# Performance work log

Hardware: AMD Instinct MI355X
Metric: run time of the kernel (lower is better)

## Reference

```python
import math
import jax, jax.numpy as jnp
import numpy as np

NUM_HEADS = 16
HEAD_DIM = 64
NB_FEATURES = 256
EPS = 1e-06
DATA_NORM = HEAD_DIM ** (-0.25)


def setup_inputs() -> dict:
    key = jax.random.key(0)
    ks = jax.random.split(key, 5)
    B, N, C = 4, 4096, 1024
    x = jax.random.normal(ks[0], (B, N, C), dtype=jnp.float32)
    w_qkv = jax.random.normal(ks[1], (C, 3 * C), dtype=jnp.float32) * (C ** -0.5)
    b_qkv = jnp.zeros((3 * C,), dtype=jnp.float32)
    w_out = jax.random.normal(ks[2], (C, C), dtype=jnp.float32) * (C ** -0.5)
    b_out = jnp.zeros((C,), dtype=jnp.float32)
    proj = jax.random.normal(ks[3], (NUM_HEADS, NB_FEATURES, HEAD_DIM), dtype=jnp.float32)
    proj = proj / jnp.linalg.norm(proj, axis=-1, keepdims=True)  # F.normalize(dim=-1)
    return {"x": x, "w_qkv": w_qkv, "b_qkv": b_qkv, "w_out": w_out, "b_out": b_out,
            "proj_matrix": proj}


def _feature_map(x, proj):
    # x: [b,h,n,d], proj: [h,m,d] -> [b,h,n,m]
    x = x * DATA_NORM
    x_proj = jnp.einsum('bhnd,hmd->bhnm', x, proj)
    sq_norms = 0.5 * jnp.sum(x * x, axis=-1, keepdims=True)
    x_proj = x_proj - sq_norms
    x_proj = x_proj - jnp.max(x_proj, axis=-1, keepdims=True)
    return (jnp.exp(x_proj) + EPS) / math.sqrt(NB_FEATURES)


def reference(x, w_qkv, b_qkv, w_out, b_out, proj_matrix):
    B, N, C = x.shape
    h, d = NUM_HEADS, HEAD_DIM
    qkv = x @ w_qkv + b_qkv                     # [B,N,3C]
    q, k, v = jnp.split(qkv, 3, axis=-1)
    to_heads = lambda z: z.reshape(B, N, h, d).transpose(0, 2, 1, 3)  # [B,h,N,d]
    q, k, v = to_heads(q), to_heads(k), to_heads(v)

    q_prime = _feature_map(q, proj_matrix)      # [B,h,N,m]
    k_prime = _feature_map(k, proj_matrix)      # [B,h,N,m]

    k_sum = jnp.sum(k_prime, axis=2)                          # [B,h,m]
    kv = jnp.einsum('bhnm,bhnd->bhmd', k_prime, v)            # [B,h,m,d]
    numerator = jnp.einsum('bhnm,bhmd->bhnd', q_prime, kv)    # [B,h,N,d]
    denominator = jnp.einsum('bhnm,bhm->bhn', q_prime, k_sum) + EPS
    out = numerator / denominator[..., None]

    out = out.transpose(0, 2, 1, 3).reshape(B, N, C)
    return out @ w_out + b_out
```

## Files before the change

kernel.cpp:

```cpp
#include <hip/hip_runtime.h>
#include <hip/hip_bf16.h>
#include <stdint.h>


#define DN 0.35355339059327379f
#define EPSF 1e-6f
#define INV_SQRT_M 0.0625f

typedef __attribute__((ext_vector_type(8))) short bf16x8;
typedef __attribute__((ext_vector_type(4))) float f32x4;

static __device__ __forceinline__ short f2bf(float f) {
    __hip_bfloat16 h = __float2bfloat16(f);
    return *(short*)&h;
}
static __device__ __forceinline__ void gload16(const void* g, void* l) {
    __builtin_amdgcn_global_load_lds(
        (const __attribute__((address_space(1))) void*)g,
        (__attribute__((address_space(3))) void*)l,
        16, 0, 0);
}

__global__ __launch_bounds__(256) void conv_x(const float* __restrict__ X,
                                              short* __restrict__ Xb) {
    int i = blockIdx.x * 256 + threadIdx.x;
    float4 v = ((const float4*)X)[i];
    short4 o;
    o.x = f2bf(v.x); o.y = f2bf(v.y); o.z = f2bf(v.z); o.w = f2bf(v.w);
    ((short4*)Xb)[i] = o;
}

__global__ __launch_bounds__(256) void convt_w(const float* __restrict__ W,
                                               short* __restrict__ WT,
                                               int K, int NN) {
    __shared__ short tile[64][66];
    int t = threadIdx.x;
    int k0 = blockIdx.y * 64, n0 = blockIdx.x * 64;
    for (int i = t; i < 4096; i += 256) {
        int r = i >> 6, c = i & 63;
        tile[r][c] = f2bf(W[(size_t)(k0 + r) * NN + n0 + c]);
    }
    __syncthreads();
    for (int i = t; i < 4096; i += 256) {
        int r = i >> 6, c = i & 63;
        WT[(size_t)(n0 + r) * K + k0 + c] = tile[c][r];
    }
}

__global__ __launch_bounds__(256) void conv_proj(const float* __restrict__ proj,
                                                 short* __restrict__ pjb) {
    int e = blockIdx.x * 256 + threadIdx.x;
    int m = (e >> 6) & 255, d = e & 63;
    int base = e & ~63;
    pjb[base + (d ^ ((m & 7) << 3))] = f2bf(proj[e]);
}

__device__ __forceinline__ void gemm_core128(const short* __restrict__ A,
                                             const short* __restrict__ BT,
                                             int rowBase, int colBase,
                                             char* smem, f32x4 acc[4][4]) {
    const int K = 1024;
    int t = threadIdx.x, lane = t & 63, w = t >> 6;
    int li = lane & 15, g = lane >> 4;
    int wm = w >> 1, wn = w & 1;

    const char* aSrc[4]; const char* bSrc[4]; int aOff[4];
#pragma unroll
    for (int c = 0; c < 4; ++c) {
        int idx = c * 256 + t;
        int r = idx >> 3, s = t & 7;
        aOff[c] = idx * 16;
        aSrc[c] = (const char*)(A + (size_t)(rowBase + r) * K + ((s ^ (r & 7)) * 8));
        bSrc[c] = (const char*)(BT + (size_t)(colBase + r) * K + ((s ^ (r & 7)) * 8));
    }
#pragma unroll
    for (int m = 0; m < 4; ++m)
#pragma unroll
        for (int n = 0; n < 4; ++n) acc[m][n] = (f32x4){0.f, 0.f, 0.f, 0.f};

#pragma unroll
    for (int c = 0; c < 4; ++c) {
        gload16(aSrc[c], smem + aOff[c]);
        gload16(bSrc[c], smem + 16384 + aOff[c]);
    }

    int swz = (li & 7) << 4;

    for (int tt = 0; tt < 16; ++tt) {
        int cur = tt & 1;
        if (tt < 15) {
            char* d = smem + (cur ^ 1) * 32768;
#pragma unroll
            for (int c = 0; c < 4; ++c) {
                gload16(aSrc[c] + (size_t)(tt + 1) * 128, d + aOff[c]);
                gload16(bSrc[c] + (size_t)(tt + 1) * 128, d + 16384 + aOff[c]);
            }
            asm volatile("s_waitcnt vmcnt(8)" ::: "memory");
        } else {
            asm volatile("s_waitcnt vmcnt(0)" ::: "memory");
        }
        __builtin_amdgcn_sched_barrier(0);
        __builtin_amdgcn_s_barrier();
        __builtin_amdgcn_sched_barrier(0);
        __builtin_amdgcn_s_setprio(1);
        const char* bA = smem + cur * 32768;
        const char* bB = bA + 16384;
#pragma unroll
        for (int ks = 0; ks < 2; ++ks) {
            int kb = ks * 64 + g * 16;
            bf16x8 af[4], bv[4];
#pragma unroll
            for (int m = 0; m < 4; ++m)
                af[m] = *(const bf16x8*)(bA + (wm * 64 + m * 16 + li) * 128 + (kb ^ swz));
#pragma unroll
            for (int n = 0; n < 4; ++n)
                bv[n] = *(const bf16x8*)(bB + (wn * 64 + n * 16 + li) * 128 + (kb ^ swz));
#pragma unroll
            for (int m = 0; m < 4; ++m)
#pragma unroll
                for (int n = 0; n < 4; ++n)
                    acc[m][n] = __builtin_amdgcn_mfma_f32_16x16x32_bf16(
                        af[m], bv[n], acc[m][n], 0, 0, 0);
        }
        __builtin_amdgcn_s_setprio(0);
        __builtin_amdgcn_sched_barrier(0);
        __builtin_amdgcn_s_barrier();
        __builtin_amdgcn_sched_barrier(0);
    }
}

__global__ __launch_bounds__(256, 2) void mfma_gemm_qkv(
        const short* __restrict__ A, const short* __restrict__ BT,
        const float* __restrict__ bias,
        short* __restrict__ Qh, short* __restrict__ Kh, short* __restrict__ Vt) {
    __shared__ __align__(16) char smem[65536];
    int t = threadIdx.x, lane = t & 63, w = t >> 6;
    int li = lane & 15, g = lane >> 4, wm = w >> 1, wn = w & 1;
    int lin = blockIdx.x;
    int sz = (lin & 7) * 384 + (lin >> 3);
    int bx = sz % 24, by = sz / 24;
    int rowBase = by * 128, colBase = bx * 128;

    f32x4 acc[4][4];
    gemm_core128(A, BT, rowBase, colBase, smem, acc);

    float bcol[4];
#pragma unroll
    for (int n = 0; n < 4; ++n) bcol[n] = bias[colBase + wn * 64 + n * 16 + li];
    int whichB = colBase >> 10;

    if (whichB == 2) {
#pragma unroll
        for (int n = 0; n < 4; ++n) {
            int gc = colBase + wn * 64 + n * 16 + li;
            int hh = (gc & 1023) >> 6, dd = gc & 63;
#pragma unroll
            for (int m = 0; m < 4; ++m) {
                int gr0 = rowBase + wm * 64 + m * 16 + g * 4;
                int b = gr0 >> 12, nn0 = gr0 & 4095;
                short4 o;
                o.x = f2bf(acc[m][n][0] + bcol[n]);
                o.y = f2bf(acc[m][n][1] + bcol[n]);
                o.z = f2bf(acc[m][n][2] + bcol[n]);
                o.w = f2bf(acc[m][n][3] + bcol[n]);
                int nsw = (nn0 & ~63) | ((nn0 & 63) ^ ((dd & 7) << 3));
                *(short4*)&Vt[((size_t)(b * 16 + hh) * 64 + dd) * 4096 + nsw] = o;
            }
        }
    } else {
        short* dst = (whichB == 0) ? Qh : Kh;
        int hh = ((colBase + wn * 64) & 1023) >> 6;
        float* wreg = (float*)(smem + w * 8704);
#pragma unroll
        for (int r = 0; r < 2; ++r) {
#pragma unroll
            for (int mi = 0; mi < 2; ++mi)
#pragma unroll
                for (int n = 0; n < 4; ++n)
#pragma unroll
                    for (int jj = 0; jj < 4; ++jj)
                        wreg[(mi * 16 + g * 4 + jj) * 68 + n * 16 + li] =
                            (acc[2 * r + mi][n][jj] + bcol[n]) * DN;
            int row = lane >> 1, h2 = lane & 1;
            int tok = rowBase + wm * 64 + r * 32 + row;
            int b = tok >> 12, nn = tok & 4095;
            size_t base = ((size_t)(b * 16 + hh) * 4096 + nn) * 64;
#pragma unroll
            for (int k = 0; k < 4; ++k) {
                float4 v0 = *(const float4*)&wreg[row * 68 + h2 * 32 + k * 8];
                float4 v1 = *(const float4*)&wreg[row * 68 + h2 * 32 + k * 8 + 4];
                bf16x8 ov;
                ov[0] = f2bf(v0.x); ov[1] = f2bf(v0.y);
                ov[2] = f2bf(v0.z); ov[3] = f2bf(v0.w);
                ov[4] = f2bf(v1.x); ov[5] = f2bf(v1.y);
                ov[6] = f2bf(v1.z); ov[7] = f2bf(v1.w);
                int dgrp = (h2 * 4 + k) ^ (tok & 7);
                *(bf16x8*)&dst[base + dgrp * 8] = ov;
            }
        }
    }
}

__global__ __launch_bounds__(256, 2) void mfma_gemm_out(
        const short* __restrict__ A, const short* __restrict__ BT,
        const float* __restrict__ bias, float* __restrict__ C) {
    __shared__ __align__(16) char smem[65536];
    int t = threadIdx.x, lane = t & 63, w = t >> 6;
    int li = lane & 15, g = lane >> 4, wm = w >> 1, wn = w & 1;
    int lin = blockIdx.x;
    int sz = (lin & 7) * 128 + (lin >> 3);
    int bx = sz & 7, by = sz >> 3;
    int rowBase = by * 128, colBase = bx * 128;

    f32x4 acc[4][4];
    gemm_core128(A, BT, rowBase, colBase, smem, acc);

    float bcol[4];
#pragma unroll
    for (int n = 0; n < 4; ++n) bcol[n] = bias[colBase + wn * 64 + n * 16 + li];
    float* wreg = (float*)(smem + w * 8704);
#pragma unroll
    for (int r = 0; r < 2; ++r) {
#pragma unroll
        for (int mi = 0; mi < 2; ++mi)
#pragma unroll
            for (int n = 0; n < 4; ++n)
#pragma unroll
                for (int jj = 0; jj < 4; ++jj)
                    wreg[(mi * 16 + g * 4 + jj) * 68 + n * 16 + li] =
                        acc[2 * r + mi][n][jj] + bcol[n];
        int row = lane >> 1, h2 = lane & 1;
        int gr = rowBase + wm * 64 + r * 32 + row;
        float* cp = C + (size_t)gr * 1024 + colBase + wn * 64 + h2 * 32;
#pragma unroll
        for (int k = 0; k < 8; ++k)
            *(float4*)&cp[k * 4] = *(const float4*)&wreg[row * 68 + h2 * 32 + k * 4];
    }
}

__global__ __launch_bounds__(256) void fmap_mfma(const short* __restrict__ Kh,
                                                 const short* __restrict__ Vt,
                                                 const short* __restrict__ pjb,
                                                 float* __restrict__ kvpart,
                                                 float* __restrict__ kspart) {
    int bh = blockIdx.y, ch = blockIdx.x, h = bh & 15;
    int t = threadIdx.x, lane = t & 63, w = t >> 6;
    int g = lane >> 4, li = lane & 15;
    __shared__ __align__(16) short pj[256 * 64];
    __shared__ __align__(16) short kt[64 * 64];
    __shared__ __align__(16) short vt[64 * 64];
    __shared__ __align__(16) short Pl[4][64 * 40];
    __shared__ __align__(16) float maxw[4][64];

    {
        const short* psrc = pjb + (size_t)h * 16384;
#pragma unroll
        for (int c2 = 0; c2 < 8; ++c2) {
            int c = 8 * w + c2;
            gload16(psrc + c * 512 + lane * 8, pj + c * 512);
        }
    }

    f32x4 acc[4][4];
#pragma unroll
    for (int i = 0; i < 4; ++i)
#pragma unroll
        for (int j = 0; j < 4; ++j) acc[i][j] = (f32x4){0.f, 0.f, 0.f, 0.f};
    float ksacc[4] = {0.f, 0.f, 0.f, 0.f};

    const short* kbase = Kh + ((size_t)bh * 4096 + ch * 512) * 64;
    const short* vbase = Vt + (size_t)bh * 64 * 4096 + ch * 512;
    int swz = (li & 7) << 4;

    for (int tile = 0; tile < 8; ++tile) {
        __syncthreads();
#pragma unroll
        for (int c2 = 0; c2 < 2; ++c2) {
            int c = 2 * w + c2;
            gload16(kbase + (size_t)(tile * 64) * 64 + c * 512 + lane * 8,
                    kt + c * 512);
            int d = 8 * c + (lane >> 3);
            gload16(vbase + (size_t)d * 4096 + tile * 64 + (lane & 7) * 8,
                    vt + c * 512);
        }
        __syncthreads();

        f32x4 sacc[4][4];
#pragma unroll
        for (int i = 0; i < 4; ++i)
#pragma unroll
            for (int j = 0; j < 4; ++j) sacc[i][j] = (f32x4){0.f, 0.f, 0.f, 0.f};
#pragma unroll
        for (int ks = 0; ks < 2; ++ks) {
            int kb = ks * 64 + g * 16;
            bf16x8 afr[4], bfr[4];
#pragma unroll
            for (int ni = 0; ni < 4; ++ni)
                afr[ni] = *(const bf16x8*)((const char*)kt +
                           (16 * ni + li) * 128 + (kb ^ swz));
#pragma unroll
            for (int mi = 0; mi < 4; ++mi)
                bfr[mi] = *(const bf16x8*)((const char*)pj +
                           (64 * w + 16 * mi + li) * 128 + (kb ^ swz));
#pragma unroll
            for (int ni = 0; ni < 4; ++ni)
#pragma unroll
                for (int mi = 0; mi < 4; ++mi)
                    sacc[ni][mi] = __builtin_amdgcn_mfma_f32_16x16x32_bf16(
                        afr[ni], bfr[mi], sacc[ni][mi], 0, 0, 0);
        }

        float mxl[4][4];
#pragma unroll
        for (int ni = 0; ni < 4; ++ni)
#pragma unroll
            for (int jj = 0; jj < 4; ++jj) {
                float m0 = fmaxf(sacc[ni][0][jj], sacc[ni][1][jj]);
                float m1 = fmaxf(sacc[ni][2][jj], sacc[ni][3][jj]);
                mxl[ni][jj] = fmaxf(m0, m1);
            }
#pragma unroll
        for (int off = 1; off <= 8; off <<= 1)
#pragma unroll
            for (int ni = 0; ni < 4; ++ni)
#pragma unroll
                for (int jj = 0; jj < 4; ++jj)
                    mxl[ni][jj] = fmaxf(mxl[ni][jj], __shfl_xor(mxl[ni][jj], off));
        if (li == 0) {
#pragma unroll
            for (int ni = 0; ni < 4; ++ni)
                *(float4*)&maxw[w][16 * ni + 4 * g] =
                    make_float4(mxl[ni][0], mxl[ni][1], mxl[ni][2], mxl[ni][3]);
        }
        __syncthreads();

#pragma unroll
        for (int hf = 0; hf < 2; ++hf) {
#pragma unroll
            for (int ni2 = 0; ni2 < 2; ++ni2) {
                int ni = 2 * hf + ni2;
                float4 a0 = *(const float4*)&maxw[0][16 * ni + 4 * g];
                float4 a1 = *(const float4*)&maxw[1][16 * ni + 4 * g];
                float4 a2 = *(const float4*)&maxw[2][16 * ni + 4 * g];
                float4 a3 = *(const float4*)&maxw[3][16 * ni + 4 * g];
                float mm[4];
                mm[0] = fmaxf(fmaxf(a0.x, a1.x), fmaxf(a2.x, a3.x));
                mm[1] = fmaxf(fmaxf(a0.y, a1.y), fmaxf(a2.y, a3.y));
                mm[2] = fmaxf(fmaxf(a0.z, a1.z), fmaxf(a2.z, a3.z));
                mm[3] = fmaxf(fmaxf(a0.w, a1.w), fmaxf(a2.w, a3.w));
#pragma unroll
                for (int mi = 0; mi < 4; ++mi) {
                    float p0 = (__expf(sacc[ni][mi][0] - mm[0]) + EPSF) * INV_SQRT_M;
                    float p1 = (__expf(sacc[ni][mi][1] - mm[1]) + EPSF) * INV_SQRT_M;
                    float p2 = (__expf(sacc[ni][mi][2] - mm[2]) + EPSF) * INV_SQRT_M;
                    float p3 = (__expf(sacc[ni][mi][3] - mm[3]) + EPSF) * INV_SQRT_M;
                    ksacc[mi] += (p0 + p1) + (p2 + p3);
                    uint32_t u0 = (uint32_t)(uint16_t)f2bf(p0) |
                                  ((uint32_t)(uint16_t)f2bf(p1) << 16);
                    uint32_t u1 = (uint32_t)(uint16_t)f2bf(p2) |
                                  ((uint32_t)(uint16_t)f2bf(p3) << 16);
                    int m_l = 16 * mi + li;
                    *(uint2*)((char*)Pl[w] + m_l * 80 + 32 * ni2 + 8 * g) =
                        make_uint2(u0, u1);
                }
            }
#pragma unroll
            for (int mi = 0; mi < 4; ++mi) {
                bf16x8 pa = *(const bf16x8*)((const char*)Pl[w] +
                             (16 * mi + li) * 80 + 16 * g);
#pragma unroll
                for (int di = 0; di < 4; ++di) {
                    bf16x8 bv = *(const bf16x8*)((const char*)vt +
                                 (16 * di + li) * 128 + ((64 * hf + 16 * g) ^ swz));
                    acc[mi][di] = __builtin_amdgcn_mfma_f32_16x16x32_bf16(
                        pa, bv, acc[mi][di], 0, 0, 0);
                }
            }
        }
    }

#pragma unroll
    for (int mi = 0; mi < 4; ++mi) {
        ksacc[mi] += __shfl_xor(ksacc[mi], 16);
        ksacc[mi] += __shfl_xor(ksacc[mi], 32);
    }
    if (lane < 16) {
#pragma unroll
        for (int mi = 0; mi < 4; ++mi)
            kspart[(bh * 8 + ch) * 256 + 64 * w + 16 * mi + li] = ksacc[mi];
    }
    float* kvb = kvpart + (size_t)(bh * 8 + ch) * 16384;
#pragma unroll
    for (int mi = 0; mi < 4; ++mi)
#pragma unroll
        for (int di = 0; di < 4; ++di) {
            int d = 16 * di + li, m0 = 64 * w + 16 * mi + 4 * g;
            *(float4*)&kvb[d * 256 + m0] =
                make_float4(acc[mi][di][0], acc[mi][di][1],
                            acc[mi][di][2], acc[mi][di][3]);
        }
}

__global__ __launch_bounds__(256) void reduce_kv(const float* __restrict__ kvpart,
                                                 const float* __restrict__ kspart,
                                                 short* __restrict__ kvsT) {
    int bh = blockIdx.y, bx = blockIdx.x, t = threadIdx.x;
    if (bx < 4) {
#pragma unroll
        for (int i = 0; i < 16; ++i) {
            int idx = t + i * 256;
            int d = 16 * bx + (idx >> 8), m = idx & 255;
            float s = 0.f;
            size_t base = ((size_t)(bh * 8) * 64 + d) * 256 + m;
#pragma unroll
            for (int c = 0; c < 8; ++c) s += kvpart[base + (size_t)c * 16384];
            int widx = (m & 128) + ((m & 127) ^ ((d & 7) << 3));
            kvsT[((size_t)bh * 80 + d) * 256 + widx] = f2bf(s);
        }
    } else {
        float s = 0.f;
#pragma unroll
        for (int c = 0; c < 8; ++c) s += kspart[((bh * 8 + c) << 8) + t];
        kvsT[((size_t)bh * 80 + 64) * 256 + t] = f2bf(s);
        for (int i = t; i < 15 * 256; i += 256) {
            int r = 65 + (i >> 8), cc = i & 255;
            kvsT[((size_t)bh * 80 + r) * 256 + cc] = 0;
        }
    }
}

__global__ __launch_bounds__(256) void contract_mfma(
        const short* __restrict__ Qh,
        const short* __restrict__ pjb,
        const short* __restrict__ kvsT,
        short* __restrict__ attn) {
    int bh = blockIdx.y, rb = blockIdx.x, h = bh & 15, b = bh >> 4;
    int t = threadIdx.x, lane = t & 63, w = t >> 6;
    __shared__ __align__(16) short qs[64 * 64];
    __shared__ __align__(16) short pj[128 * 64];
    __shared__ __align__(16) short Pl[64 * 128];
    __shared__ __align__(16) short kvl[80 * 128];

    {
        const short* src = Qh + ((size_t)bh * 4096 + rb * 64) * 64;
#pragma unroll
        for (int c2 = 0; c2 < 2; ++c2) {
            int c = 2 * w + c2;
            gload16(src + (c * 8 + (lane >> 3)) * 64 + (lane & 7) * 8,
                    qs + c * 512);
        }
    }

    f32x4 acc5[5];
#pragma unroll
    for (int i = 0; i < 5; ++i) acc5[i] = (f32x4){0.f, 0.f, 0.f, 0.f};

    int g = lane >> 4, li = lane & 15;

    for (int half = 0; half < 2; ++half) {
        __syncthreads();
        const short* psrc = pjb + (size_t)h * 16384 + half * 8192;
#pragma unroll
        for (int c2 = 0; c2 < 4; ++c2) {
            int c = 4 * w + c2;
            gload16(psrc + (c * 8 + (lane >> 3)) * 64 + (lane & 7) * 8,
                    pj + c * 512);
        }
        const short* ksrc = kvsT + (size_t)bh * 80 * 256 + half * 128;
#pragma unroll
        for (int c2 = 0; c2 < 5; ++c2) {
            int c = 5 * w + c2;
            gload16(ksrc + (c * 4 + (lane >> 4)) * 256 + (lane & 15) * 8,
                    kvl + c * 512);
        }
        __syncthreads();

        f32x4 sacc[2][4];
#pragma unroll
        for (int mi = 0; mi < 2; ++mi)
#pragma unroll
            for (int ni = 0; ni < 4; ++ni) sacc[mi][ni] = (f32x4){0.f, 0.f, 0.f, 0.f};
#pragma unroll
        for (int ks = 0; ks < 2; ++ks) {
            int kbyte = ks * 64 + g * 16;
            bf16x8 afr[2], bfr[4];
#pragma unroll
            for (int mi = 0; mi < 2; ++mi) {
                int mr = 32 * w + 16 * mi + li;
                afr[mi] = *(const bf16x8*)((const char*)pj +
                           mr * 128 + (kbyte ^ ((mr & 7) << 4)));
            }
#pragma unroll
            for (int ni = 0; ni < 4; ++ni) {
                int qr = 16 * ni + li;
                bfr[ni] = *(const bf16x8*)((const char*)qs +
                           qr * 128 + (kbyte ^ ((qr & 7) << 4)));
            }
#pragma unroll
            for (int mi = 0; mi < 2; ++mi)
#pragma unroll
                for (int ni = 0; ni < 4; ++ni)
                    sacc[mi][ni] = __builtin_amdgcn_mfma_f32_16x16x32_bf16(
                        afr[mi], bfr[ni], sacc[mi][ni], 0, 0, 0);
        }

#pragma unroll
        for (int mi = 0; mi < 2; ++mi) {
            int m0 = 32 * w + 16 * mi + 4 * g;
#pragma unroll
            for (int ni = 0; ni < 4; ++ni) {
                int row = 16 * ni + li;
                float e0 = (__expf(sacc[mi][ni][0]) + EPSF) * INV_SQRT_M;
                float e1 = (__expf(sacc[mi][ni][1]) + EPSF) * INV_SQRT_M;
                float e2 = (__expf(sacc[mi][ni][2]) + EPSF) * INV_SQRT_M;
                float e3 = (__expf(sacc[mi][ni][3]) + EPSF) * INV_SQRT_M;
                uint32_t u0 = (uint32_t)(uint16_t)f2bf(e0) |
                              ((uint32_t)(uint16_t)f2bf(e1) << 16);
                uint32_t u1 = (uint32_t)(uint16_t)f2bf(e2) |
                              ((uint32_t)(uint16_t)f2bf(e3) << 16);
                int byte = row * 256 + ((m0 * 2) ^ ((row & 7) << 4));
                *(uint2*)((char*)Pl + byte) = make_uint2(u0, u1);
            }
        }
        __syncthreads();

        int rowA = 16 * w + li;
        int abase = rowA * 256;
        int asw = (rowA & 7) << 4;
#pragma unroll
        for (int ks = 0; ks < 4; ++ks) {
            int kbyte = ks * 64 + g * 16;
            bf16x8 pa = *(const bf16x8*)((const char*)Pl + abase + (kbyte ^ asw));
#pragma unroll
            for (int ni = 0; ni < 5; ++ni) {
                int rowB = 16 * ni + li;
                bf16x8 bv = *(const bf16x8*)((const char*)kvl +
                             rowB * 256 + (kbyte ^ ((rowB & 7) << 4)));
                acc5[ni] = __builtin_amdgcn_mfma_f32_16x16x32_bf16(
                    pa, bv, acc5[ni], 0, 0, 0);
            }
        }
    }

    float dj[4];
#pragma unroll
    for (int jj = 0; jj < 4; ++jj)
        dj[jj] = __shfl(acc5[4][jj], lane & 48) + EPSF;
#pragma unroll
    for (int ni = 0; ni < 4; ++ni) {
        int d = 16 * ni + li;
#pragma unroll
        for (int jj = 0; jj < 4; ++jj) {
            int n = rb * 64 + 16 * w + 4 * g + jj;
            attn[((size_t)b * 4096 + n) * 1024 + h * 64 + d] =
                f2bf(acc5[ni][jj] / dj[jj]);
        }
    }
}

extern "C" void kernel_launch(void* const* d_in, const int* in_sizes, int n_in,
                              void* d_out, int out_size, void* d_ws, size_t ws_size,
                              hipStream_t stream) {
    const float* x      = (const float*)d_in[0];
    const float* w_qkv  = (const float*)d_in[1];
    const float* b_qkv  = (const float*)d_in[2];
    const float* w_out  = (const float*)d_in[3];
    const float* b_out  = (const float*)d_in[4];
    const float* proj   = (const float*)d_in[5];
    float* out = (float*)d_out;

    char* w = (char*)d_ws;
    short* xb     = (short*)(w);
    short* wqT    = (short*)(w + 33554432);
    short* wOT    = (short*)(w + 39845888);
    short* Qh     = (short*)(w + 41943040);
    short* Kh     = (short*)(w + 75497472);
    short* Vt     = (short*)(w + 109051904);
    float* kvpart = (float*)(w);
    float* kspart = (float*)(w + 142606336);
    short* kvsT   = (short*)(w + 143130624);
    short* pjb    = (short*)(w + 145752064);
    short* attn   = Kh;

    conv_x<<<dim3(16384), 256, 0, stream>>>(x, xb);
    convt_w<<<dim3(48, 16), 256, 0, stream>>>(w_qkv, wqT, 1024, 3072);
    convt_w<<<dim3(16, 16), 256, 0, stream>>>(w_out, wOT, 1024, 1024);
    conv_proj<<<dim3(1024), 256, 0, stream>>>(proj, pjb);
    mfma_gemm_qkv<<<dim3(3072), 256, 0, stream>>>(xb, wqT, b_qkv, Qh, Kh, Vt);
    fmap_mfma<<<dim3(8, 64), 256, 0, stream>>>(Kh, Vt, pjb, kvpart, kspart);
    reduce_kv<<<dim3(5, 64), 256, 0, stream>>>(kvpart, kspart, kvsT);
    contract_mfma<<<dim3(64, 64), 256, 0, stream>>>(Qh, pjb, kvsT, attn);
    mfma_gemm_out<<<dim3(1024), 256, 0, stream>>>(attn, wOT, b_out, out);
}
```

Before: 333.3 us.

## Prefetch K/V tiles via registers, double rows per contract block, drop GEMM swizzle

In fmap_mfma, the next K/V tile is loaded into registers while the current tile is computed, then written to LDS after a barrier, so global load latency overlaps MFMA work. contract_mfma now handles 128 query rows per block (two row groups), loading projection and kv tiles once per half and reusing them, which halves the grid and the redundant pj/kv loads. The block-index swizzle in both GEMMs is removed in favour of plain row-major tile order, which may reduce L2 reuse. Register pressure and LDS usage rise in the modified kernels.

After: 321.7 us. 1.04x faster.

```diff
diff --git a/kernel.cpp b/kernel.cpp
--- a/kernel.cpp
+++ b/kernel.cpp
@@ -137,8 +137,7 @@
     int t = threadIdx.x, lane = t & 63, w = t >> 6;
     int li = lane & 15, g = lane >> 4, wm = w >> 1, wn = w & 1;
     int lin = blockIdx.x;
-    int sz = (lin & 7) * 384 + (lin >> 3);
-    int bx = sz % 24, by = sz / 24;
+    int bx = lin % 24, by = lin / 24;
     int rowBase = by * 128, colBase = bx * 128;
 
     f32x4 acc[4][4];
@@ -208,8 +207,7 @@
     int t = threadIdx.x, lane = t & 63, w = t >> 6;
     int li = lane & 15, g = lane >> 4, wm = w >> 1, wn = w & 1;
     int lin = blockIdx.x;
-    int sz = (lin & 7) * 128 + (lin >> 3);
-    int bx = sz & 7, by = sz >> 3;
+    int bx = lin & 7, by = lin >> 3;
     int rowBase = by * 128, colBase = bx * 128;
 
     f32x4 acc[4][4];
@@ -252,6 +250,9 @@
     __shared__ __align__(16) short Pl[4][64 * 40];
     __shared__ __align__(16) float maxw[4][64];
 
+    const short* kbase = Kh + ((size_t)bh * 4096 + ch * 512) * 64;
+    const short* vbase = Vt + (size_t)bh * 64 * 4096 + ch * 512;
+
     {
         const short* psrc = pjb + (size_t)h * 16384;
 #pragma unroll
@@ -259,7 +260,15 @@
             int c = 8 * w + c2;
             gload16(psrc + c * 512 + lane * 8, pj + c * 512);
         }
-    }
+#pragma unroll
+        for (int c2 = 0; c2 < 2; ++c2) {
+            int c = 2 * w + c2;
+            gload16(kbase + c * 512 + lane * 8, kt + c * 512);
+            int d = 8 * c + (lane >> 3);
+            gload16(vbase + (size_t)d * 4096 + (lane & 7) * 8, vt + c * 512);
+        }
+    }
+    __syncthreads();
 
     f32x4 acc[4][4];
 #pragma unroll
@@ -268,22 +277,19 @@
         for (int j = 0; j < 4; ++j) acc[i][j] = (f32x4){0.f, 0.f, 0.f, 0.f};
     float ksacc[4] = {0.f, 0.f, 0.f, 0.f};
 
-    const short* kbase = Kh + ((size_t)bh * 4096 + ch * 512) * 64;
-    const short* vbase = Vt + (size_t)bh * 64 * 4096 + ch * 512;
     int swz = (li & 7) << 4;
 
     for (int tile = 0; tile < 8; ++tile) {
-        __syncthreads();
-#pragma unroll
-        for (int c2 = 0; c2 < 2; ++c2) {
-            int c = 2 * w + c2;
-            gload16(kbase + (size_t)(tile * 64) * 64 + c * 512 + lane * 8,
-                    kt + c * 512);
-            int d = 8 * c + (lane >> 3);
-            gload16(vbase + (size_t)d * 4096 + tile * 64 + (lane & 7) * 8,
-                    vt + c * 512);
-        }
-        __syncthreads();
+        bf16x8 rk0, rk1, rv0, rv1;
+        if (tile < 7) {
+            int c0 = 2 * w, c1 = 2 * w + 1;
+            size_t kof = (size_t)((tile + 1) * 64) * 64;
+            rk0 = *(const bf16x8*)(kbase + kof + c0 * 512 + lane * 8);
+            rk1 = *(const bf16x8*)(kbase + kof + c1 * 512 + lane * 8);
+            int d0 = 8 * c0 + (lane >> 3), d1 = 8 * c1 + (lane >> 3);
+            rv0 = *(const bf16x8*)(vbase + (size_t)d0 * 4096 + (tile + 1) * 64 + (lane & 7) * 8);
+            rv1 = *(const bf16x8*)(vbase + (size_t)d1 * 4096 + (tile + 1) * 64 + (lane & 7) * 8);
+        }
 
         f32x4 sacc[4][4];
 #pragma unroll
@@ -377,6 +383,15 @@
                 }
             }
         }
+        __syncthreads();
+        if (tile < 7) {
+            int c0 = 2 * w, c1 = 2 * w + 1;
+            *(bf16x8*)((char*)kt + c0 * 1024 + lane * 16) = rk0;
+            *(bf16x8*)((char*)kt + c1 * 1024 + lane * 16) = rk1;
+            *(bf16x8*)((char*)vt + c0 * 1024 + lane * 16) = rv0;
+            *(bf16x8*)((char*)vt + c1 * 1024 + lane * 16) = rv1;
+            __syncthreads();
+        }
     }
 
 #pragma unroll
@@ -436,29 +451,30 @@
         short* __restrict__ attn) {
     int bh = blockIdx.y, rb = blockIdx.x, h = bh & 15, b = bh >> 4;
     int t = threadIdx.x, lane = t & 63, w = t >> 6;
-    __shared__ __align__(16) short qs[64 * 64];
+    __shared__ __align__(16) short qs[128 * 64];
     __shared__ __align__(16) short pj[128 * 64];
     __shared__ __align__(16) short Pl[64 * 128];
     __shared__ __align__(16) short kvl[80 * 128];
 
     {
-        const short* src = Qh + ((size_t)bh * 4096 + rb * 64) * 64;
-#pragma unroll
-        for (int c2 = 0; c2 < 2; ++c2) {
-            int c = 2 * w + c2;
+        const short* src = Qh + ((size_t)bh * 4096 + rb * 128) * 64;
+#pragma unroll
+        for (int c2 = 0; c2 < 4; ++c2) {
+            int c = 4 * w + c2;
             gload16(src + (c * 8 + (lane >> 3)) * 64 + (lane & 7) * 8,
                     qs + c * 512);
         }
     }
 
-    f32x4 acc5[5];
-#pragma unroll
-    for (int i = 0; i < 5; ++i) acc5[i] = (f32x4){0.f, 0.f, 0.f, 0.f};
+    f32x4 acc5[2][5];
+#pragma unroll
+    for (int rg = 0; rg < 2; ++rg)
+#pragma unroll
+        for (int i = 0; i < 5; ++i) acc5[rg][i] = (f32x4){0.f, 0.f, 0.f, 0.f};
 
     int g = lane >> 4, li = lane & 15;
 
     for (int half = 0; half < 2; ++half) {
-        __syncthreads();
         const short* psrc = pjb + (size_t)h * 16384 + half * 8192;
 #pragma unroll
         for (int c2 = 0; c2 < 4; ++c2) {
@@ -475,85 +491,92 @@
         }
         __syncthreads();
 
-        f32x4 sacc[2][4];
-#pragma unroll
-        for (int mi = 0; mi < 2; ++mi)
-#pragma unroll
-            for (int ni = 0; ni < 4; ++ni) sacc[mi][ni] = (f32x4){0.f, 0.f, 0.f, 0.f};
-#pragma unroll
-        for (int ks = 0; ks < 2; ++ks) {
-            int kbyte = ks * 64 + g * 16;
-            bf16x8 afr[2], bfr[4];
+#pragma unroll
+        for (int rg = 0; rg < 2; ++rg) {
+            f32x4 sacc[2][4];
+#pragma unroll
+            for (int mi = 0; mi < 2; ++mi)
+#pragma unroll
+                for (int ni = 0; ni < 4; ++ni) sacc[mi][ni] = (f32x4){0.f, 0.f, 0.f, 0.f};
+#pragma unroll
+            for (int ks = 0; ks < 2; ++ks) {
+                int kbyte = ks * 64 + g * 16;
+                bf16x8 afr[2], bfr[4];
+#pragma unroll
+                for (int mi = 0; mi < 2; ++mi) {
+                    int mr = 32 * w + 16 * mi + li;
+                    afr[mi] = *(const bf16x8*)((const char*)pj +
+                               mr * 128 + (kbyte ^ ((mr & 7) << 4)));
+                }
+#pragma unroll
+                for (int ni = 0; ni < 4; ++ni) {
+                    int qr = rg * 64 + 16 * ni + li;
+                    bfr[ni] = *(const bf16x8*)((const char*)qs +
+                               qr * 128 + (kbyte ^ ((qr & 7) << 4)));
+                }
+#pragma unroll
+                for (int mi = 0; mi < 2; ++mi)
+#pragma unroll
+                    for (int ni = 0; ni < 4; ++ni)
+                        sacc[mi][ni] = __builtin_amdgcn_mfma_f32_16x16x32_bf16(
+                            afr[mi], bfr[ni], sacc[mi][ni], 0, 0, 0);
+            }
+
 #pragma unroll
             for (int mi = 0; mi < 2; ++mi) {
-                int mr = 32 * w + 16 * mi + li;
-                afr[mi] = *(const bf16x8*)((const char*)pj +
-                           mr * 128 + (kbyte ^ ((mr & 7) << 4)));
-            }
-#pragma unroll
-            for (int ni = 0; ni < 4; ++ni) {
-                int qr = 16 * ni + li;
-                bfr[ni] = *(const bf16x8*)((const char*)qs +
-                           qr * 128 + (kbyte ^ ((qr & 7) << 4)));
-            }
-#pragma unroll
-            for (int mi = 0; mi < 2; ++mi)
-#pragma unroll
-                for (int ni = 0; ni < 4; ++ni)
-                    sacc[mi][ni] = __builtin_amdgcn_mfma_f32_16x16x32_bf16(
-                        afr[mi], bfr[ni], sacc[mi][ni], 0, 0, 0);
-        }
-
-#pragma unroll
-        for (int mi = 0; mi < 2; ++mi) {
-            int m0 = 32 * w + 16 * mi + 4 * g;
-#pragma unroll
-            for (int ni = 0; ni < 4; ++ni) {
-                int row = 16 * ni + li;
-                float e0 = (__expf(sacc[mi][ni][0]) + EPSF) * INV_SQRT_M;
-                float e1 = (__expf(sacc[mi][ni][1]) + EPSF) * INV_SQRT_M;
-                float e2 = (__expf(sacc[mi][ni][2]) + EPSF) * INV_SQRT_M;
-                float e3 = (__expf(sacc[mi][ni][3]) + EPSF) * INV_SQRT_M;
-                uint32_t u0 = (uint32_t)(uint16_t)f2bf(e0) |
-                              ((uint32_t)(uint16_t)f2bf(e1) << 16);
-                uint32_t u1 = (uint32_t)(uint16_t)f2bf(e2) |
-                              ((uint32_t)(uint16_t)f2bf(e3) << 16);
-                int byte = row * 256 + ((m0 * 2) ^ ((row & 7) << 4));
-                *(uint2*)((char*)Pl + byte) = make_uint2(u0, u1);
-            }
-        }
-        __syncthreads();
-
-        int rowA = 16 * w + li;
-        int abase = rowA * 256;
-        int asw = (rowA & 7) << 4;
-#pragma unroll
-        for (int ks = 0; ks < 4; ++ks) {
-            int kbyte = ks * 64 + g * 16;
-            bf16x8 pa = *(const bf16x8*)((const char*)Pl + abase + (kbyte ^ asw));
-#pragma unroll
-            for (int ni = 0; ni < 5; ++ni) {
-                int rowB = 16 * ni + li;
-                bf16x8 bv = *(const bf16x8*)((const char*)kvl +
-                             rowB * 256 + (kbyte ^ ((rowB & 7) << 4)));
-                acc5[ni] = __builtin_amdgcn_mfma_f32_16x16x32_bf16(
-                    pa, bv, acc5[ni], 0, 0, 0);
-            }
-        }
-    }
-
-    float dj[4];
-#pragma unroll
-    for (int jj = 0; jj < 4; ++jj)
-        dj[jj] = __shfl(acc5[4][jj], lane & 48) + EPSF;
-#pragma unroll
-    for (int ni = 0; ni < 4; ++ni) {
-        int d = 16 * ni + li;
-#pragma unroll
-        for (int jj = 0; jj < 4; ++jj) {
-            int n = rb * 64 + 16 * w + 4 * g + jj;
-            attn[((size_t)b * 4096 + n) * 1024 + h * 64 + d] =
-                f2bf(acc5[ni][jj] / dj[jj]);
+                int m0 = 32 * w + 16 * mi + 4 * g;
+#pragma unroll
+                for (int ni = 0; ni < 4; ++ni) {
+                    int row = 16 * ni + li;
+                    float e0 = (__expf(sacc[mi][ni][0]) + EPSF) * INV_SQRT_M;
+                    float e1 = (__expf(sacc[mi][ni][1]) + EPSF) * INV_SQRT_M;
+                    float e2 = (__expf(sacc[mi][ni][2]) + EPSF) * INV_SQRT_M;
+                    float e3 = (__expf(sacc[mi][ni][3]) + EPSF) * INV_SQRT_M;
+                    uint32_t u0 = (uint32_t)(uint16_t)f2bf(e0) |
+                                  ((uint32_t)(uint16_t)f2bf(e1) << 16);
+                    uint32_t u1 = (uint32_t)(uint16_t)f2bf(e2) |
+                                  ((uint32_t)(uint16_t)f2bf(e3) << 16);
+                    int byte = row * 256 + ((m0 * 2) ^ ((row & 7) << 4));
+                    *(uint2*)((char*)Pl + byte) = make_uint2(u0, u1);
+                }
+            }
+            __syncthreads();
+
+            int rowA = 16 * w + li;
+            int abase = rowA * 256;
+            int asw = (rowA & 7) << 4;
+#pragma unroll
+            for (int ks = 0; ks < 4; ++ks) {
+                int kbyte = ks * 64 + g * 16;
+                bf16x8 pa = *(const bf16x8*)((const char*)Pl + abase + (kbyte ^ asw));
+#pragma unroll
+                for (int ni = 0; ni < 5; ++ni) {
+                    int rowB = 16 * ni + li;
+                    bf16x8 bv = *(const bf16x8*)((const char*)kvl +
+                                 rowB * 256 + (kbyte ^ ((rowB & 7) << 4)));
+                    acc5[rg][ni] = __builtin_amdgcn_mfma_f32_16x16x32_bf16(
+                        pa, bv, acc5[rg][ni], 0, 0, 0);
+                }
+            }
+            __syncthreads();
+        }
+    }
+
+#pragma unroll
+    for (int rg = 0; rg < 2; ++rg) {
+        float dj[4];
+#pragma unroll
+        for (int jj = 0; jj < 4; ++jj)
+            dj[jj] = __shfl(acc5[rg][4][jj], lane & 48) + EPSF;
+#pragma unroll
+        for (int ni = 0; ni < 4; ++ni) {
+            int d = 16 * ni + li;
+#pragma unroll
+            for (int jj = 0; jj < 4; ++jj) {
+                int n = rb * 128 + rg * 64 + 16 * w + 4 * g + jj;
+                attn[((size_t)b * 4096 + n) * 1024 + h * 64 + d] =
+                    f2bf(acc5[rg][ni][jj] / dj[jj]);
+            }
         }
     }
 }
@@ -589,6 +612,6 @@
     mfma_gemm_qkv<<<dim3(3072), 256, 0, stream>>>(xb, wqT, b_qkv, Qh, Kh, Vt);
     fmap_mfma<<<dim3(8, 64), 256, 0, stream>>>(Kh, Vt, pjb, kvpart, kspart);
     reduce_kv<<<dim3(5, 64), 256, 0, stream>>>(kvpart, kspart, kvsT);
-    contract_mfma<<<dim3(64, 64), 256, 0, stream>>>(Qh, pjb, kvsT, attn);
+    contract_mfma<<<dim3(32, 64), 256, 0, stream>>>(Qh, pjb, kvsT, attn);
     mfma_gemm_out<<<dim3(1024), 256, 0, stream>>>(attn, wOT, b_out, out);
 }
```
